# Kernel optimization log

Measured on AMD Instinct MI355X. Metric: run time of the kernel, lower is better.

## Reference

```python
import jax, jax.numpy as jnp
import numpy as np

B, V, E = 1024, 50257, 128

def setup_inputs() -> dict:
    key = jax.random.key(0)
    k1, k2, k3, k4 = jax.random.split(key, 4)
    # xs: one-hot focus-word vectors [B, V]
    focus_ids = jax.random.randint(k1, (B,), 0, V)
    xs = jnp.zeros((B, V), dtype=jnp.float32).at[jnp.arange(B), focus_ids].set(1.0)
    metric = jax.random.normal(k2, (E, E), dtype=jnp.float32)
    EMBEDM = jax.random.normal(k3, (V, E), dtype=jnp.float32)
    NEGEMBEDM = jax.random.normal(k4, (V, E), dtype=jnp.float32)
    return {"xs": xs, "metric": metric, "EMBEDM": EMBEDM, "NEGEMBEDM": NEGEMBEDM}

def reference(xs, metric, EMBEDM, NEGEMBEDM):
    # xs @ EMBEDM : one-hot matmul == row gather, but kept as GEMM to match original math
    xsembeds = xs @ EMBEDM                              # [B, E]
    # dots(vs, ws, metric) = (vs @ metric) @ ws.T
    scores = (xsembeds @ metric) @ NEGEMBEDM.T          # [B, V]
    return jax.nn.log_softmax(scores, axis=1)
```

## Files before the change

### kernel.cpp

```cpp
#include <hip/hip_runtime.h>
#include <hip/hip_bf16.h>
#include <math.h>

#define B_ROWS 1024
#define V_COLS 50257
#define E_DIM  128
#define BM     128
#define BN     128
#define NNB    393
#define VPAD   (NNB * BN)
#define N4     (V_COLS * E_DIM / 4)
#define N4P    (VPAD * E_DIM / 4)

typedef __attribute__((ext_vector_type(8))) short short8;
typedef __attribute__((ext_vector_type(4))) float floatx4;

static __device__ __forceinline__ unsigned short f2bf(float x) {
    union { float f; unsigned int u; } c; c.f = x;
    unsigned int u = c.u;
    unsigned int r = u + 0x7fffu + ((u >> 16) & 1u);
    return (unsigned short)(r >> 16);
}

__global__ void find_idx_kernel(const float4* __restrict__ xs4, int* __restrict__ idx) {
    long i = (long)blockIdx.x * blockDim.x + threadIdx.x;
    const long n4 = (long)B_ROWS * V_COLS / 4;
    if (i >= n4) return;
    float4 v = xs4[i];
    float vals[4] = {v.x, v.y, v.z, v.w};
    #pragma unroll
    for (int c = 0; c < 4; ++c) {
        if (vals[c] != 0.0f) {
            long f = 4 * i + c;
            int b = (int)(f / V_COLS);
            idx[b] = (int)(f - (long)b * V_COLS);
        }
    }
}

__global__ void cvt_bf16_kernel(const float4* __restrict__ src, ushort4* __restrict__ dst) {
    int i = blockIdx.x * blockDim.x + threadIdx.x;
    if (i >= N4P) return;
    ushort4 o;
    if (i < N4) {
        float4 v = src[i];
        o.x = f2bf(v.x); o.y = f2bf(v.y); o.z = f2bf(v.z); o.w = f2bf(v.w);
    } else {
        o.x = 0; o.y = 0; o.z = 0; o.w = 0;
    }
    dst[i] = o;
}

__global__ void compute_t_kernel(const float* __restrict__ EMB, const float* __restrict__ metric,
                                 const int* __restrict__ idx, unsigned short* __restrict__ t) {
    __shared__ float erow[E_DIM];
    int b = blockIdx.x, tid = threadIdx.x;
    int id = idx[b];
    erow[tid] = EMB[(long)id * E_DIM + tid];
    __syncthreads();
    float acc = 0.f;
    #pragma unroll 16
    for (int k = 0; k < E_DIM; ++k) acc += erow[k] * metric[k * E_DIM + tid];
    t[b * E_DIM + tid] = f2bf(acc);
}

template <bool WRITE_OUT>
__global__ __launch_bounds__(256) void gemm_kernel(const unsigned short* __restrict__ t,
                                                   const unsigned short* __restrict__ neg,
                                                   float2* __restrict__ partials,
                                                   const float* __restrict__ lse,
                                                   float* __restrict__ out) {
    __shared__ __align__(16) unsigned char smem[128 * 132 * 4];
    __shared__ float2 stats[2][128];
    __shared__ float lsev[128];

    const int tid  = threadIdx.x;
    const int lane = tid & 63, wave = tid >> 6;
    const int l16  = lane & 15, q = lane >> 4;
    const int wm   = wave >> 1, wn = wave & 1;
    const int mbase = blockIdx.y * BM;
    const int nbase = blockIdx.x * BN;

    if (WRITE_OUT && tid < 128) lsev[tid] = lse[mbase + tid];

    uint4* ldsA = (uint4*)smem;
    uint4* ldsB = (uint4*)(smem + 32768);
    const uint4* srcA = (const uint4*)(t + (size_t)mbase * E_DIM);
    const uint4* srcB = (const uint4*)(neg + (size_t)nbase * E_DIM);
    #pragma unroll
    for (int it = 0; it < 8; ++it) {
        int idx = it * 256 + tid;
        int r = idx >> 4, c = idx & 15;
        int d = (r << 4) + (c ^ (r & 15));
        ldsA[d] = srcA[idx];
        ldsB[d] = srcB[idx];
    }
    __syncthreads();

    floatx4 acc[4][4];
    #pragma unroll
    for (int i = 0; i < 4; ++i)
        #pragma unroll
        for (int j = 0; j < 4; ++j) acc[i][j] = (floatx4){0, 0, 0, 0};

    #pragma unroll
    for (int ks = 0; ks < 4; ++ks) {
        short8 af[4], bfr[4];
        #pragma unroll
        for (int mf = 0; mf < 4; ++mf) {
            int row = wm * 64 + mf * 16 + l16;
            af[mf] = *(const short8*)&ldsA[(row << 4) + ((ks * 4 + q) ^ (row & 15))];
        }
        #pragma unroll
        for (int nt = 0; nt < 4; ++nt) {
            int row = wn * 64 + nt * 16 + l16;
            bfr[nt] = *(const short8*)&ldsB[(row << 4) + ((ks * 4 + q) ^ (row & 15))];
        }
        #pragma unroll
        for (int mf = 0; mf < 4; ++mf)
            #pragma unroll
            for (int nt = 0; nt < 4; ++nt)
                acc[mf][nt] = __builtin_amdgcn_mfma_f32_16x16x32_bf16(af[mf], bfr[nt], acc[mf][nt], 0, 0, 0);
    }


    if (!WRITE_OUT) {
        #pragma unroll
        for (int mf = 0; mf < 4; ++mf) {
            #pragma unroll
            for (int r = 0; r < 4; ++r) {
                bool valid[4];
                #pragma unroll
                for (int nt = 0; nt < 4; ++nt)
                    valid[nt] = (nbase + wn * 64 + nt * 16 + l16) < V_COLS;
                float mx = -INFINITY;
                #pragma unroll
                for (int nt = 0; nt < 4; ++nt)
                    if (valid[nt]) mx = fmaxf(mx, acc[mf][nt][r]);
                #pragma unroll
                for (int d = 1; d < 16; d <<= 1) mx = fmaxf(mx, __shfl_xor(mx, d, 16));
                float s = 0.f;
                #pragma unroll
                for (int nt = 0; nt < 4; ++nt)
                    if (valid[nt]) s += __expf(acc[mf][nt][r] - mx);
                #pragma unroll
                for (int d = 1; d < 16; d <<= 1) s += __shfl_xor(s, d, 16);
                if (l16 == 0) stats[wn][wm * 64 + mf * 16 + q * 4 + r] = make_float2(mx, s);
            }
        }
        __syncthreads();
        if (tid < 128) {
            float2 p0 = stats[0][tid], p1 = stats[1][tid];
            float mm = fmaxf(p0.x, p1.x);
            float ss = p0.y * __expf(p0.x - mm) + p1.y * __expf(p1.x - mm);
            partials[(long)(mbase + tid) * NNB + blockIdx.x] = make_float2(mm, ss);
        }
    } else {
        __syncthreads();
        float* sbuf = (float*)smem;
        #pragma unroll
        for (int mf = 0; mf < 4; ++mf)
            #pragma unroll
            for (int nt = 0; nt < 4; ++nt)
                #pragma unroll
                for (int r = 0; r < 4; ++r)
                    sbuf[(wm * 64 + mf * 16 + q * 4 + r) * 132 + wn * 64 + nt * 16 + l16] = acc[mf][nt][r];
        __syncthreads();
        #pragma unroll 4
        for (int it = 0; it < 64; ++it) {
            int i = it * 256 + tid;
            int r = i >> 7, c = i & 127;
            int col = nbase + c;
            if (col < V_COLS)
                out[(size_t)(mbase + r) * V_COLS + col] = sbuf[r * 132 + c] - lsev[r];
        }
    }
}

__global__ void merge_lse_kernel(const float2* __restrict__ partials, float* __restrict__ lse) {
    int b = blockIdx.x;
    int tid = threadIdx.x;
    float m = -INFINITY, s = 0.f;
    for (int i = tid; i < NNB; i += 256) {
        float2 p = partials[(long)b * NNB + i];
        if (p.x > m) { s = s * __expf(m - p.x) + p.y; m = p.x; }
        else         { s += p.y * __expf(p.x - m); }
    }
    __shared__ float sm[256], ss[256];
    sm[tid] = m; ss[tid] = s;
    __syncthreads();
    for (int off = 128; off > 0; off >>= 1) {
        if (tid < off) {
            float m1 = sm[tid], s1 = ss[tid];
            float m2 = sm[tid + off], s2 = ss[tid + off];
            float mm = fmaxf(m1, m2);
            sm[tid] = mm;
            ss[tid] = s1 * __expf(m1 - mm) + s2 * __expf(m2 - mm);
        }
        __syncthreads();
    }
    if (tid == 0) lse[b] = sm[0] + __logf(ss[0]);
}

extern "C" void kernel_launch(void* const* d_in, const int* in_sizes, int n_in,
                              void* d_out, int out_size, void* d_ws, size_t ws_size,
                              hipStream_t stream) {
    const float* xs     = (const float*)d_in[0];
    const float* metric = (const float*)d_in[1];
    const float* EMB    = (const float*)d_in[2];
    const float* NEG    = (const float*)d_in[3];
    float* out = (float*)d_out;

    char* ws = (char*)d_ws;
    int*            idx      = (int*)ws;
    unsigned short* t        = (unsigned short*)(ws + 4096);
    unsigned short* neg16    = (unsigned short*)(ws + 266240);
    float2*         partials = (float2*)(ws + 13144064);
    float*          lse      = (float*)(ws + 16363520);

    {
        long n4 = (long)B_ROWS * V_COLS / 4;
        int blocks = (int)((n4 + 255) / 256);
        find_idx_kernel<<<blocks, 256, 0, stream>>>((const float4*)xs, idx);
    }
    cvt_bf16_kernel<<<(N4P + 255) / 256, 256, 0, stream>>>((const float4*)NEG, (ushort4*)neg16);
    compute_t_kernel<<<B_ROWS, E_DIM, 0, stream>>>(EMB, metric, idx, t);
    gemm_kernel<false><<<dim3(NNB, B_ROWS / BM), 256, 0, stream>>>(t, neg16, partials, nullptr, nullptr);
    merge_lse_kernel<<<B_ROWS, 256, 0, stream>>>(partials, lse);
    gemm_kernel<true><<<dim3(NNB, B_ROWS / BM), 256, 0, stream>>>(t, neg16, partials, lse, out);
}
```

Baseline: 467.0 us.

## Keep A fragments in registers across column tiles and store output directly

Drops LDS staging: each block loads its row-block fragments of t into registers once and iterates over three column tiles, loading NEG fragments directly from global memory. The statistics pass keeps an online running max/sum across tiles, reducing the partials count, and the output pass writes results straight from MFMA accumulators instead of transposing through LDS. The goal is to cut LDS traffic, synchronisation and block count, at the cost of less coalesced output stores and higher register pressure.

```diff
diff --git a/kernel.cpp b/kernel.cpp
--- a/kernel.cpp
+++ b/kernel.cpp
@@ -5,10 +5,10 @@
 #define B_ROWS 1024
 #define V_COLS 50257
 #define E_DIM  128
-#define BM     128
-#define BN     128
-#define NNB    393
-#define VPAD   (NNB * BN)
+#define NTILES 393
+#define VPAD   (NTILES * 128)
+#define TPB    3
+#define NX     131
 #define N4     (V_COLS * E_DIM / 4)
 #define N4P    (VPAD * E_DIM / 4)
 
@@ -65,114 +65,127 @@
 }
 
 template <bool WRITE_OUT>
-__global__ __launch_bounds__(256) void gemm_kernel(const unsigned short* __restrict__ t,
-                                                   const unsigned short* __restrict__ neg,
-                                                   float2* __restrict__ partials,
-                                                   const float* __restrict__ lse,
-                                                   float* __restrict__ out) {
-    __shared__ __align__(16) unsigned char smem[128 * 132 * 4];
+__global__ __launch_bounds__(256, 2) void gemm_kernel(const unsigned short* __restrict__ t,
+                                                      const unsigned short* __restrict__ neg,
+                                                      float2* __restrict__ partials,
+                                                      const float* __restrict__ lse,
+                                                      float* __restrict__ out) {
     __shared__ float2 stats[2][128];
-    __shared__ float lsev[128];
 
     const int tid  = threadIdx.x;
     const int lane = tid & 63, wave = tid >> 6;
     const int l16  = lane & 15, q = lane >> 4;
     const int wm   = wave >> 1, wn = wave & 1;
-    const int mbase = blockIdx.y * BM;
-    const int nbase = blockIdx.x * BN;
-
-    if (WRITE_OUT && tid < 128) lsev[tid] = lse[mbase + tid];
-
-    uint4* ldsA = (uint4*)smem;
-    uint4* ldsB = (uint4*)(smem + 32768);
-    const uint4* srcA = (const uint4*)(t + (size_t)mbase * E_DIM);
-    const uint4* srcB = (const uint4*)(neg + (size_t)nbase * E_DIM);
+    const int mbase = blockIdx.x * 128;
+    const int tile0 = blockIdx.y * TPB;
+
+    short8 af[4][4];
     #pragma unroll
-    for (int it = 0; it < 8; ++it) {
-        int idx = it * 256 + tid;
-        int r = idx >> 4, c = idx & 15;
-        int d = (r << 4) + (c ^ (r & 15));
-        ldsA[d] = srcA[idx];
-        ldsB[d] = srcB[idx];
-    }
-    __syncthreads();
-
-    floatx4 acc[4][4];
-    #pragma unroll
-    for (int i = 0; i < 4; ++i)
-        #pragma unroll
-        for (int j = 0; j < 4; ++j) acc[i][j] = (floatx4){0, 0, 0, 0};
-
-    #pragma unroll
-    for (int ks = 0; ks < 4; ++ks) {
-        short8 af[4], bfr[4];
-        #pragma unroll
-        for (int mf = 0; mf < 4; ++mf) {
-            int row = wm * 64 + mf * 16 + l16;
-            af[mf] = *(const short8*)&ldsA[(row << 4) + ((ks * 4 + q) ^ (row & 15))];
-        }
+    for (int mf = 0; mf < 4; ++mf) {
+        const unsigned short* arow = t + (size_t)(mbase + wm * 64 + mf * 16 + l16) * E_DIM + q * 8;
+        #pragma unroll
+        for (int ks = 0; ks < 4; ++ks)
+            af[mf][ks] = *(const short8*)(arow + ks * 32);
+    }
+
+    float lsev[4][4];
+    float rm[4][4], rs[4][4];
+    if (WRITE_OUT) {
+        #pragma unroll
+        for (int mf = 0; mf < 4; ++mf)
+            #pragma unroll
+            for (int r = 0; r < 4; ++r)
+                lsev[mf][r] = lse[mbase + wm * 64 + mf * 16 + q * 4 + r];
+    } else {
+        #pragma unroll
+        for (int mf = 0; mf < 4; ++mf)
+            #pragma unroll
+            for (int r = 0; r < 4; ++r) { rm[mf][r] = -1e30f; rs[mf][r] = 0.f; }
+    }
+
+    for (int it = 0; it < TPB; ++it) {
+        const int colbase = (tile0 + it) * 128 + wn * 64;
+
+        short8 bf[4][4];
         #pragma unroll
         for (int nt = 0; nt < 4; ++nt) {
-            int row = wn * 64 + nt * 16 + l16;
-            bfr[nt] = *(const short8*)&ldsB[(row << 4) + ((ks * 4 + q) ^ (row & 15))];
-        }
-        #pragma unroll
-        for (int mf = 0; mf < 4; ++mf)
-            #pragma unroll
-            for (int nt = 0; nt < 4; ++nt)
-                acc[mf][nt] = __builtin_amdgcn_mfma_f32_16x16x32_bf16(af[mf], bfr[nt], acc[mf][nt], 0, 0, 0);
-    }
-
-
-    if (!WRITE_OUT) {
-        #pragma unroll
-        for (int mf = 0; mf < 4; ++mf) {
-            #pragma unroll
-            for (int r = 0; r < 4; ++r) {
-                bool valid[4];
+            const unsigned short* brow = neg + (size_t)(colbase + nt * 16 + l16) * E_DIM + q * 8;
+            #pragma unroll
+            for (int ks = 0; ks < 4; ++ks)
+                bf[nt][ks] = *(const short8*)(brow + ks * 32);
+        }
+
+        floatx4 acc[4][4];
+        #pragma unroll
+        for (int mf = 0; mf < 4; ++mf)
+            #pragma unroll
+            for (int nt = 0; nt < 4; ++nt) acc[mf][nt] = (floatx4){0, 0, 0, 0};
+
+        #pragma unroll
+        for (int ks = 0; ks < 4; ++ks)
+            #pragma unroll
+            for (int mf = 0; mf < 4; ++mf)
                 #pragma unroll
                 for (int nt = 0; nt < 4; ++nt)
-                    valid[nt] = (nbase + wn * 64 + nt * 16 + l16) < V_COLS;
-                float mx = -INFINITY;
+                    acc[mf][nt] = __builtin_amdgcn_mfma_f32_16x16x32_bf16(af[mf][ks], bf[nt][ks], acc[mf][nt], 0, 0, 0);
+
+        if (WRITE_OUT) {
+            #pragma unroll
+            for (int nt = 0; nt < 4; ++nt) {
+                const int col = colbase + nt * 16 + l16;
+                if (col < V_COLS) {
+                    #pragma unroll
+                    for (int mf = 0; mf < 4; ++mf) {
+                        const size_t rb = (size_t)(mbase + wm * 64 + mf * 16 + q * 4) * V_COLS + col;
+                        #pragma unroll
+                        for (int r = 0; r < 4; ++r)
+                            out[rb + (size_t)r * V_COLS] = acc[mf][nt][r] - lsev[mf][r];
+                    }
+                }
+            }
+        } else {
+            bool ok[4];
+            #pragma unroll
+            for (int nt = 0; nt < 4; ++nt) ok[nt] = (colbase + nt * 16 + l16) < V_COLS;
+            #pragma unroll
+            for (int mf = 0; mf < 4; ++mf)
                 #pragma unroll
-                for (int nt = 0; nt < 4; ++nt)
-                    if (valid[nt]) mx = fmaxf(mx, acc[mf][nt][r]);
+                for (int r = 0; r < 4; ++r) {
+                    float m = rm[mf][r], s = rs[mf][r];
+                    #pragma unroll
+                    for (int nt = 0; nt < 4; ++nt) {
+                        float v = acc[mf][nt][r];
+                        float mm = ok[nt] ? fmaxf(m, v) : m;
+                        s = s * __expf(m - mm) + (ok[nt] ? __expf(v - mm) : 0.f);
+                        m = mm;
+                    }
+                    rm[mf][r] = m; rs[mf][r] = s;
+                }
+        }
+    }
+
+    if (!WRITE_OUT) {
+        #pragma unroll
+        for (int mf = 0; mf < 4; ++mf)
+            #pragma unroll
+            for (int r = 0; r < 4; ++r) {
+                float m = rm[mf][r], s = rs[mf][r];
                 #pragma unroll
-                for (int d = 1; d < 16; d <<= 1) mx = fmaxf(mx, __shfl_xor(mx, d, 16));
-                float s = 0.f;
-                #pragma unroll
-                for (int nt = 0; nt < 4; ++nt)
-                    if (valid[nt]) s += __expf(acc[mf][nt][r] - mx);
-                #pragma unroll
-                for (int d = 1; d < 16; d <<= 1) s += __shfl_xor(s, d, 16);
-                if (l16 == 0) stats[wn][wm * 64 + mf * 16 + q * 4 + r] = make_float2(mx, s);
+                for (int d = 1; d < 16; d <<= 1) {
+                    float m2 = __shfl_xor(m, d, 16);
+                    float s2 = __shfl_xor(s, d, 16);
+                    float mm = fmaxf(m, m2);
+                    s = s * __expf(m - mm) + s2 * __expf(m2 - mm);
+                    m = mm;
+                }
+                if (l16 == 0) stats[wn][wm * 64 + mf * 16 + q * 4 + r] = make_float2(m, s);
             }
-        }
         __syncthreads();
         if (tid < 128) {
             float2 p0 = stats[0][tid], p1 = stats[1][tid];
             float mm = fmaxf(p0.x, p1.x);
             float ss = p0.y * __expf(p0.x - mm) + p1.y * __expf(p1.x - mm);
-            partials[(long)(mbase + tid) * NNB + blockIdx.x] = make_float2(mm, ss);
-        }
-    } else {
-        __syncthreads();
-        float* sbuf = (float*)smem;
-        #pragma unroll
-        for (int mf = 0; mf < 4; ++mf)
-            #pragma unroll
-            for (int nt = 0; nt < 4; ++nt)
-                #pragma unroll
-                for (int r = 0; r < 4; ++r)
-                    sbuf[(wm * 64 + mf * 16 + q * 4 + r) * 132 + wn * 64 + nt * 16 + l16] = acc[mf][nt][r];
-        __syncthreads();
-        #pragma unroll 4
-        for (int it = 0; it < 64; ++it) {
-            int i = it * 256 + tid;
-            int r = i >> 7, c = i & 127;
-            int col = nbase + c;
-            if (col < V_COLS)
-                out[(size_t)(mbase + r) * V_COLS + col] = sbuf[r * 132 + c] - lsev[r];
+            partials[(long)(mbase + tid) * NX + blockIdx.y] = make_float2(mm, ss);
         }
     }
 }
@@ -180,11 +193,12 @@
 __global__ void merge_lse_kernel(const float2* __restrict__ partials, float* __restrict__ lse) {
     int b = blockIdx.x;
     int tid = threadIdx.x;
-    float m = -INFINITY, s = 0.f;
-    for (int i = tid; i < NNB; i += 256) {
-        float2 p = partials[(long)b * NNB + i];
-        if (p.x > m) { s = s * __expf(m - p.x) + p.y; m = p.x; }
-        else         { s += p.y * __expf(p.x - m); }
+    float m = -1e30f, s = 0.f;
+    for (int i = tid; i < NX; i += 256) {
+        float2 p = partials[(long)b * NX + i];
+        float mm = fmaxf(m, p.x);
+        s = s * __expf(m - mm) + p.y * __expf(p.x - mm);
+        m = mm;
     }
     __shared__ float sm[256], ss[256];
     sm[tid] = m; ss[tid] = s;
@@ -216,7 +230,7 @@
     unsigned short* t        = (unsigned short*)(ws + 4096);
     unsigned short* neg16    = (unsigned short*)(ws + 266240);
     float2*         partials = (float2*)(ws + 13144064);
-    float*          lse      = (float*)(ws + 16363520);
+    float*          lse      = (float*)(ws + 14217216);
 
     {
         long n4 = (long)B_ROWS * V_COLS / 4;
@@ -225,7 +239,7 @@
     }
     cvt_bf16_kernel<<<(N4P + 255) / 256, 256, 0, stream>>>((const float4*)NEG, (ushort4*)neg16);
     compute_t_kernel<<<B_ROWS, E_DIM, 0, stream>>>(EMB, metric, idx, t);
-    gemm_kernel<false><<<dim3(NNB, B_ROWS / BM), 256, 0, stream>>>(t, neg16, partials, nullptr, nullptr);
+    gemm_kernel<false><<<dim3(8, NX), 256, 0, stream>>>(t, neg16, partials, nullptr, nullptr);
     merge_lse_kernel<<<B_ROWS, 256, 0, stream>>>(partials, lse);
-    gemm_kernel<true><<<dim3(NNB, B_ROWS / BM), 256, 0, stream>>>(t, neg16, partials, lse, out);
-}
+    gemm_kernel<true><<<dim3(8, NX), 256, 0, stream>>>(t, neg16, partials, lse, out);
+}
```

Result: slower. 511.1 us (+9.4%).
